# Kernel optimization log

Hardware: AMD Instinct MI355X
Metric: run time of the kernel (lower is better)

## Reference

```python
import jax, jax.numpy as jnp
import numpy as np

N, D, K = 10000, 784, 16          # nodes, input feat dim, num_neighbors
E = N * (K - 1)                   # edges
H = 128                           # hidden width in all MLPs
SIZES = [784, 128, 2]             # node_sizes


def setup_inputs() -> dict:
    key = jax.random.key(0)
    ks = jax.random.split(key, 24)
    w = lambda k, shape: jax.random.normal(k, shape, jnp.float32) * 0.02
    inp = {
        "x": jax.random.normal(ks[0], (N, D), jnp.float32),
        "edge_attr": jax.random.uniform(ks[1], (E, 1), jnp.float32),
        "idxs": jax.random.randint(ks[2], (N, K - 1), 0, N, dtype=jnp.int32),
    }
    # Layer 1: in=784, msg_size=784, out=128
    inp["l1_msg_w1"] = w(ks[3], (D + 1, H));      inp["l1_msg_b1"] = jnp.zeros((H,), jnp.float32)
    inp["l1_msg_w2"] = w(ks[4], (H, D));          inp["l1_msg_b2"] = jnp.zeros((D,), jnp.float32)
    inp["l1_node_w1"] = w(ks[5], (D + D, H));     inp["l1_node_b1"] = jnp.zeros((H,), jnp.float32)
    inp["l1_node_w2"] = w(ks[6], (H, 128));       inp["l1_node_b2"] = jnp.zeros((128,), jnp.float32)
    # Layer 2: in=128, msg_size=128, out=2
    inp["l2_msg_w1"] = w(ks[7], (128 + 1, H));    inp["l2_msg_b1"] = jnp.zeros((H,), jnp.float32)
    inp["l2_msg_w2"] = w(ks[8], (H, 128));        inp["l2_msg_b2"] = jnp.zeros((128,), jnp.float32)
    inp["l2_node_w1"] = w(ks[9], (128 + 128, H)); inp["l2_node_b1"] = jnp.zeros((H,), jnp.float32)
    inp["l2_node_w2"] = w(ks[10], (H, 2));        inp["l2_node_b2"] = jnp.zeros((2,), jnp.float32)
    return inp


def _mlp(x, w1, b1, w2, b2):
    return jax.nn.relu(x @ w1 + b1) @ w2 + b2


def _node_layer(x, src, edge_attr,
                mw1, mb1, mw2, mb2, nw1, nb1, nw2, nb2):
    # message over edges: cat(x[src], edge_attr) -> MLP   [E, msg_size]
    msg = _mlp(jnp.concatenate([x[src], edge_attr], axis=1), mw1, mb1, mw2, mb2)
    # scatter_mean by src index (faithful to the original, which uses index=src)
    sums = jax.ops.segment_sum(msg, src, num_segments=N)
    cnt = jax.ops.segment_sum(jnp.ones((src.shape[0], 1), msg.dtype), src, num_segments=N)
    agg = jnp.where(cnt > 0, sums / jnp.maximum(cnt, 1.0), 0.0)
    # node update: cat(x, agg_msg) -> MLP
    return _mlp(jnp.concatenate([x, agg], axis=1), nw1, nb1, nw2, nb2)


def reference(x, edge_attr, idxs,
              l1_msg_w1, l1_msg_b1, l1_msg_w2, l1_msg_b2,
              l1_node_w1, l1_node_b1, l1_node_w2, l1_node_b2,
              l2_msg_w1, l2_msg_b1, l2_msg_w2, l2_msg_b2,
              l2_node_w1, l2_node_b1, l2_node_w2, l2_node_b2):
    src = idxs.reshape(-1)  # [E]; dst is unused by the original message computation
    h = _node_layer(x, src, edge_attr,
                    l1_msg_w1, l1_msg_b1, l1_msg_w2, l1_msg_b2,
                    l1_node_w1, l1_node_b1, l1_node_w2, l1_node_b2)
    proj = _node_layer(h, src, edge_attr,
                       l2_msg_w1, l2_msg_b1, l2_msg_w2, l2_msg_b2,
                       l2_node_w1, l2_node_b1, l2_node_w2, l2_node_b2)  # [N, 2]
    # vectorized per-neighbor squared distances (replaces the nested python loop)
    neigh = proj[idxs]                                   # [N, K-1, 2]
    d = jnp.sum((proj[:, None, :] - neigh) ** 2, axis=-1)  # [N, K-1]
    return d.reshape(-1, 1)                              # [N*(K-1), 1]
```

## Files before the change

kernel.cpp:

```cpp
#include <hip/hip_runtime.h>

#define N_NODES 10000
#define E_EDGES 150000
#define KNB     15
#define EBLOCKS 587
#define GEMMB   626
#define KPAD    832
#define PLSTR   212992
#define CFSTR   13312

typedef unsigned short u16;
typedef __bf16 bf16x8 __attribute__((ext_vector_type(8)));
typedef float  f32x4  __attribute__((ext_vector_type(4)));
typedef unsigned short u16x8 __attribute__((ext_vector_type(8)));

__device__ __forceinline__ void split3(float a, u16& h, u16& m, u16& l) {
    unsigned u = __float_as_uint(a);
    unsigned t = u + 0x7FFFu + ((u >> 16) & 1u);
    h = (u16)(t >> 16);
    float r1 = a - __uint_as_float(t & 0xFFFF0000u);
    unsigned u1 = __float_as_uint(r1);
    m = (u16)(u1 >> 16);
    float r2 = r1 - __uint_as_float(u1 & 0xFFFF0000u);
    l = (u16)(__float_as_uint(r2) >> 16);
}

__global__ void count_kernel(const int* __restrict__ idxs, int* __restrict__ cnt, int e) {
    int i = blockIdx.x * blockDim.x + threadIdx.x;
    if (i < e) atomicAdd(&cnt[idxs[i]], 1);
}

__device__ __forceinline__
void gemm_tile2(const float* __restrict__ A, int K,
                const float* __restrict__ Blo, const float* __restrict__ Bhi, int ldB,
                float* __restrict__ C, int ldC, int M,
                int rowBlk, int colBlk) {
    __shared__ float As2[16][34];
    __shared__ float Bs2[16][64];
    int tid = threadIdx.x;
    int tn  = tid & 15, tm = tid >> 4;
    int arow = tid >> 3, acB = (tid & 7) << 1;
    int brow = tid >> 4, bcol = (tid & 15) << 2;
    int rowBase = rowBlk * 32, colBase = colBlk * 64;

    bool half = (Bhi != nullptr) && (colBase >= 128);
    const float* B = half ? Bhi : Blo;
    int bj = colBase - (half ? 128 : 0) + bcol;

    float2 av; float4 bv;
    auto loadA = [&](int k0, float2& dst) {
        int gr = rowBase + arow;
        if (gr < M) dst = *(const float2*)(A + (size_t)gr * K + k0 + acB);
        else { dst.x = dst.y = 0.f; }
    };
    auto loadB = [&](int k0, float4& dst) {
        dst = *(const float4*)(B + (size_t)(k0 + brow) * ldB + bj);
    };
    loadA(0, av); loadB(0, bv);

    float acc[2][4] = {};
    for (int k0 = 0; k0 < K; k0 += 16) {
        __syncthreads();
        As2[acB + 0][arow] = av.x; As2[acB + 1][arow] = av.y;
        *(float4*)&Bs2[brow][bcol] = bv;
        __syncthreads();
        if (k0 + 16 < K) { loadA(k0 + 16, av); loadB(k0 + 16, bv); }
#pragma unroll
        for (int k = 0; k < 16; ++k) {
            float4 b = *(const float4*)&Bs2[k][tn << 2];
            float2 a = *(const float2*)&As2[k][tm << 1];
            acc[0][0] = fmaf(a.x, b.x, acc[0][0]); acc[0][1] = fmaf(a.x, b.y, acc[0][1]);
            acc[0][2] = fmaf(a.x, b.z, acc[0][2]); acc[0][3] = fmaf(a.x, b.w, acc[0][3]);
            acc[1][0] = fmaf(a.y, b.x, acc[1][0]); acc[1][1] = fmaf(a.y, b.y, acc[1][1]);
            acc[1][2] = fmaf(a.y, b.z, acc[1][2]); acc[1][3] = fmaf(a.y, b.w, acc[1][3]);
        }
    }
#pragma unroll
    for (int i = 0; i < 2; ++i) {
        int row = rowBase + tm * 2 + i;
        if (row >= M) continue;
#pragma unroll
        for (int j = 0; j < 4; ++j)
            C[(size_t)row * ldC + colBase + (tn << 2) + j] = acc[i][j];
    }
}

__global__ __launch_bounds__(256)
void scanfold_kernel(const float* __restrict__ mw2, const float* __restrict__ mb2,
                     const float* __restrict__ nw1, const float* __restrict__ nb2,
                     const float* __restrict__ nw2,
                     const float* __restrict__ m2w1, const float* __restrict__ m2b1,
                     const float* __restrict__ m2w2, const float* __restrict__ m2b2,
                     const float* __restrict__ n2w1, const float* __restrict__ n2b1,
                     float* __restrict__ M1, float* __restrict__ M2,
                     float* __restrict__ WH,
                     float* __restrict__ v1, float* __restrict__ v2,
                     float* __restrict__ bu2, float* __restrict__ bx2,
                     const int* __restrict__ cnt, int* __restrict__ eoff,
                     float* __restrict__ maskv, int* __restrict__ fillc,
                     const float* __restrict__ mw1, u16* __restrict__ Bt) {
    int b = blockIdx.x;
    if (b >= 41) {
        __shared__ float Lt[KPAD][17];
        int b2 = b - 41;
        int colBase = b2 * 16;
        const float* S = (colBase < 128) ? mw1 : nw1;
        int sc = colBase & 127;
        int tid = threadIdx.x;
        for (int i = 0; i < 52; ++i) {
            int row = (tid >> 4) + i * 16;
            Lt[row][tid & 15] = (row < 784) ? S[(size_t)row * 128 + sc + (tid & 15)] : 0.f;
        }
        __syncthreads();
        int col = tid >> 4, o = tid & 15;
        size_t dbase = (size_t)(colBase + col) * KPAD;
        for (int o2 = o; o2 < 104; o2 += 16) {
            u16 hs[8], ms[8], ls[8];
#pragma unroll
            for (int e = 0; e < 8; ++e) split3(Lt[o2 * 8 + e][col], hs[e], ms[e], ls[e]);
            auto pk = [](const u16* s) {
                uint4 v;
                v.x = s[0] | ((unsigned)s[1] << 16); v.y = s[2] | ((unsigned)s[3] << 16);
                v.z = s[4] | ((unsigned)s[5] << 16); v.w = s[6] | ((unsigned)s[7] << 16);
                return v;
            };
            *(uint4*)(Bt +           dbase + o2 * 8) = pk(hs);
            *(uint4*)(Bt + PLSTR   + dbase + o2 * 8) = pk(ms);
            *(uint4*)(Bt + 2*PLSTR + dbase + o2 * 8) = pk(ls);
        }
        return;
    }
    if (b == 0) {
        __shared__ int ssum[256];
        int tid = threadIdx.x;
        const int CH = 40;
        int base = tid * CH;
        int v[CH]; int s = 0;
#pragma unroll
        for (int q = 0; q < CH; ++q) {
            int i = base + q;
            v[q] = (i < N_NODES) ? cnt[i] : 0;
            s += v[q];
        }
        ssum[tid] = s;
        __syncthreads();
        for (int off = 1; off < 256; off <<= 1) {
            int t = (tid >= off) ? ssum[tid - off] : 0;
            __syncthreads();
            ssum[tid] += t;
            __syncthreads();
        }
        int ex = ssum[tid] - s;
#pragma unroll
        for (int q = 0; q < CH; ++q) {
            int i = base + q;
            if (i < N_NODES) {
                eoff[i]  = ex;
                maskv[i] = (v[q] > 0) ? 1.f : 0.f;
                fillc[i] = 0;
                ex += v[q];
            }
        }
        return;
    }
    b -= 1;
    if (b < 8) {
        gemm_tile2(mw2, 784, nw1 + 784 * 128, nullptr, 128, M1, 128, 128, b >> 1, b & 1);
    } else if (b < 16) {
        int t = b - 8;
        gemm_tile2(m2w2, 128, n2w1 + 128 * 128, nullptr, 128, M2, 128, 128, t >> 1, t & 1);
    } else if (b < 32) {
        int t = b - 16;
        gemm_tile2(nw2, 128, m2w1, n2w1, 128, WH, 256, 128, t >> 2, t & 3);
    } else {
        __shared__ float red[256];
        int t  = (b - 32) >> 1;
        int j  = ((b - 32) & 1) * 64 + (threadIdx.x & 63);
        int kq = threadIdx.x >> 6;
        const float* bvec; const float* Bv; const float* add; float* out; int Kv;
        if (t == 0)      { bvec = mb2;  Bv = nw1 + 784 * 128;  add = nullptr; out = v1;  Kv = 784; }
        else if (t == 1) { bvec = m2b2; Bv = n2w1 + 128 * 128; add = nullptr; out = v2;  Kv = 128; }
        else if (t == 2) { bvec = nb2;  Bv = m2w1;             add = m2b1;    out = bu2; Kv = 128; }
        else             { bvec = nb2;  Bv = n2w1;             add = n2b1;    out = bx2; Kv = 128; }
        float acc = 0.f;
        for (int k = kq; k < Kv; k += 4) acc = fmaf(bvec[k], Bv[k * 128 + j], acc);
        red[threadIdx.x] = acc;
        __syncthreads();
        if (threadIdx.x < 64) {
            float tot = red[threadIdx.x] + red[threadIdx.x + 64] +
                        red[threadIdx.x + 128] + red[threadIdx.x + 192];
            out[j] = tot + (add ? add[j] : 0.f);
        }
    }
}

#define MF(a, b, c) __builtin_amdgcn_mfma_f32_16x16x32_bf16((a), (b), (c), 0, 0, 0)

__device__ __forceinline__
void gemm_mfma(const float* __restrict__ A, const u16* __restrict__ Bt,
               const float* __restrict__ biasLo, const float* __restrict__ biasHi,
               const float* __restrict__ vhi, const float* __restrict__ rowmask,
               float* __restrict__ C, int gb) {
    __shared__ u16 As[3][2][2][64][8];
    const int tid  = threadIdx.x;
    const int lane = tid & 63, w = tid >> 6;
    const int rb = gb >> 1, cb = gb & 1;
    const int rowBase = rb * 32, colBase = cb * 128;
    u16* const AsB = &As[0][0][0][0][0];

    const int skt = w >> 1, srf = w & 1;
    const int aoff = skt * 32 + ((lane >> 4) << 3);
    int arow = rowBase + srf * 16 + (lane & 15);
    if (arow > N_NODES - 1) arow = N_NODES - 1;
    const float* Ap = A + (size_t)arow * 784;
    u16* aDst = AsB + skt * 1024 + srf * 512 + (lane << 3);

    const u16* Bp = Bt + (size_t)(colBase + w * 32 + (lane & 15)) * KPAD
                       + ((lane >> 4) << 3);

    float4 av0, av1;
    u16x8 a3h, a3m, a3l;

#define ALOAD(k0) { int kk = (k0) + aoff; \
    if (kk < 784) { av0 = *(const float4*)(Ap + kk); av1 = *(const float4*)(Ap + kk + 4); } \
    else { av0.x=av0.y=av0.z=av0.w=0.f; av1 = av0; } }
#define ASPLIT() { u16 h, m, l; \
    split3(av0.x, h, m, l); a3h[0] = h; a3m[0] = m; a3l[0] = l; \
    split3(av0.y, h, m, l); a3h[1] = h; a3m[1] = m; a3l[1] = l; \
    split3(av0.z, h, m, l); a3h[2] = h; a3m[2] = m; a3l[2] = l; \
    split3(av0.w, h, m, l); a3h[3] = h; a3m[3] = m; a3l[3] = l; \
    split3(av1.x, h, m, l); a3h[4] = h; a3m[4] = m; a3l[4] = l; \
    split3(av1.y, h, m, l); a3h[5] = h; a3m[5] = m; a3l[5] = l; \
    split3(av1.z, h, m, l); a3h[6] = h; a3m[6] = m; a3l[6] = l; \
    split3(av1.w, h, m, l); a3h[7] = h; a3m[7] = m; a3l[7] = l; }

#define BDECL(S) bf16x8 S##h00, S##h01, S##h10, S##h11, \
                        S##m00, S##m01, S##m10, S##m11, \
                        S##l00, S##l01, S##l10, S##l11;
#define BLOAD(S, k0) \
    S##h00 = *(const bf16x8*)(Bp + (k0)); \
    S##h01 = *(const bf16x8*)(Bp + (k0) + CFSTR); \
    S##h10 = *(const bf16x8*)(Bp + (k0) + 32); \
    S##h11 = *(const bf16x8*)(Bp + (k0) + CFSTR + 32); \
    S##m00 = *(const bf16x8*)(Bp + (k0) + PLSTR); \
    S##m01 = *(const bf16x8*)(Bp + (k0) + PLSTR + CFSTR); \
    S##m10 = *(const bf16x8*)(Bp + (k0) + PLSTR + 32); \
    S##m11 = *(const bf16x8*)(Bp + (k0) + PLSTR + CFSTR + 32); \
    S##l00 = *(const bf16x8*)(Bp + (k0) + 2*PLSTR); \
    S##l01 = *(const bf16x8*)(Bp + (k0) + 2*PLSTR + CFSTR); \
    S##l10 = *(const bf16x8*)(Bp + (k0) + 2*PLSTR + 32); \
    S##l11 = *(const bf16x8*)(Bp + (k0) + 2*PLSTR + CFSTR + 32);

#define DOMFMA(S) { \
    {  \
        bf16x8 a0h = *(const bf16x8*)(aFr); \
        bf16x8 a1h = *(const bf16x8*)(aFr + 512); \
        bf16x8 a0m = *(const bf16x8*)(aFr + 2048); \
        bf16x8 a1m = *(const bf16x8*)(aFr + 2560); \
        bf16x8 a0l = *(const bf16x8*)(aFr + 4096); \
        bf16x8 a1l = *(const bf16x8*)(aFr + 4608); \
        acc00 = MF(a0h, S##h00, acc00); acc01 = MF(a0h, S##h01, acc01); \
        acc10 = MF(a1h, S##h00, acc10); acc11 = MF(a1h, S##h01, acc11); \
        acc00 = MF(a0m, S##h00, acc00); acc01 = MF(a0m, S##h01, acc01); \
        acc10 = MF(a1m, S##h00, acc10); acc11 = MF(a1m, S##h01, acc11); \
        acc00 = MF(a0l, S##h00, acc00); acc01 = MF(a0l, S##h01, acc01); \
        acc10 = MF(a1l, S##h00, acc10); acc11 = MF(a1l, S##h01, acc11); \
        acc00 = MF(a0h, S##m00, acc00); acc01 = MF(a0h, S##m01, acc01); \
        acc10 = MF(a1h, S##m00, acc10); acc11 = MF(a1h, S##m01, acc11); \
        acc00 = MF(a0m, S##m00, acc00); acc01 = MF(a0m, S##m01, acc01); \
        acc10 = MF(a1m, S##m00, acc10); acc11 = MF(a1m, S##m01, acc11); \
        acc00 = MF(a0h, S##l00, acc00); acc01 = MF(a0h, S##l01, acc01); \
        acc10 = MF(a1h, S##l00, acc10); acc11 = MF(a1h, S##l01, acc11); \
    } \
    {  \
        bf16x8 a0h = *(const bf16x8*)(aFr + 1024); \
        bf16x8 a1h = *(const bf16x8*)(aFr + 1536); \
        bf16x8 a0m = *(const bf16x8*)(aFr + 3072); \
        bf16x8 a1m = *(const bf16x8*)(aFr + 3584); \
        bf16x8 a0l = *(const bf16x8*)(aFr + 5120); \
        bf16x8 a1l = *(const bf16x8*)(aFr + 5632); \
        acc00 = MF(a0h, S##h10, acc00); acc01 = MF(a0h, S##h11, acc01); \
        acc10 = MF(a1h, S##h10, acc10); acc11 = MF(a1h, S##h11, acc11); \
        acc00 = MF(a0m, S##h10, acc00); acc01 = MF(a0m, S##h11, acc01); \
        acc10 = MF(a1m, S##h10, acc10); acc11 = MF(a1m, S##h11, acc11); \
        acc00 = MF(a0l, S##h10, acc00); acc01 = MF(a0l, S##h11, acc01); \
        acc10 = MF(a1l, S##h10, acc10); acc11 = MF(a1l, S##h11, acc11); \
        acc00 = MF(a0h, S##m10, acc00); acc01 = MF(a0h, S##m11, acc01); \
        acc10 = MF(a1h, S##m10, acc10); acc11 = MF(a1h, S##m11, acc11); \
        acc00 = MF(a0m, S##m10, acc00); acc01 = MF(a0m, S##m11, acc01); \
        acc10 = MF(a1m, S##m10, acc10); acc11 = MF(a1m, S##m11, acc11); \
        acc00 = MF(a0h, S##l10, acc00); acc01 = MF(a0h, S##l11, acc01); \
        acc10 = MF(a1h, S##l10, acc10); acc11 = MF(a1h, S##l11, acc11); \
    } }

#define ITER(CUR, NXT, T) { \
    __syncthreads(); \
    *(u16x8*)(aDst)        = a3h; \
    *(u16x8*)(aDst + 2048) = a3m; \
    *(u16x8*)(aDst + 4096) = a3l; \
    __syncthreads(); \
    if ((T) < 12) { ALOAD(((T) + 1) << 6) BLOAD(NXT, ((T) + 1) << 6) } \
    DOMFMA(CUR) \
    if ((T) < 12) { ASPLIT() } }

    f32x4 acc00 = {0.f, 0.f, 0.f, 0.f};
    f32x4 acc01 = acc00, acc10 = acc00, acc11 = acc00;

    const u16* aFr = AsB + (lane << 3);

    BDECL(p) BDECL(q)
    ALOAD(0) ASPLIT()
    BLOAD(p, 0)

    ITER(p, q, 0)  ITER(q, p, 1)  ITER(p, q, 2)  ITER(q, p, 3)
    ITER(p, q, 4)  ITER(q, p, 5)  ITER(p, q, 6)  ITER(q, p, 7)
    ITER(p, q, 8)  ITER(q, p, 9)  ITER(p, q, 10) ITER(q, p, 11)
    ITER(p, q, 12)

#undef ITER
#undef DOMFMA
#undef BLOAD
#undef BDECL
#undef ALOAD
#undef ASPLIT

    const float* bias = cb ? biasHi : biasLo;
#define EPI(rf, cf, ACC) { \
        const int col = colBase + w * 32 + (cf) * 16 + (lane & 15); \
        const int cj  = col & 127; \
        const float bb = bias[cj]; \
        const float vh = cb ? vhi[cj] : 0.f; \
        const int rbase = rowBase + (rf) * 16 + ((lane >> 4) << 2); \
        _Pragma("unroll") \
        for (int rr = 0; rr < 4; ++rr) { \
            int row = rbase + rr; \
            if (row < N_NODES) { \
                float v = ACC[rr] + bb; \
                if (cb) v = fmaf(rowmask[row], vh, v); \
                C[(size_t)row * 256 + col] = v; \
            } } }
    EPI(0, 0, acc00) EPI(0, 1, acc01) EPI(1, 0, acc10) EPI(1, 1, acc11)
#undef EPI
}

__global__ __launch_bounds__(256, 1)
void fillgemm_kernel(const int* __restrict__ idxs, const float* __restrict__ ea,
                     const int* __restrict__ eoff, int* __restrict__ fillc,
                     float* __restrict__ eas,
                     const float* __restrict__ A, const u16* __restrict__ Bt,
                     const float* __restrict__ biasLo, const float* __restrict__ biasHi,
                     const float* __restrict__ vhi, const float* __restrict__ rowmask,
                     float* __restrict__ C) {
    int gb = blockIdx.x;
    if (gb < GEMMB) {
        gemm_mfma(A, Bt, biasLo, biasHi, vhi, rowmask, C, gb);
        return;
    }
    int i = (gb - GEMMB) * 256 + threadIdx.x;
    if (i < E_EDGES) {
        int s = idxs[i];
        int p = atomicAdd(&fillc[s], 1);
        eas[eoff[s] + p] = ea[i];
    }
}

__global__ __launch_bounds__(512, 4)
void tail16_kernel(const float* __restrict__ UX1, const float* __restrict__ w1last,
                   const float* __restrict__ eas, const int* __restrict__ eoff,
                   const int* __restrict__ cnt, const float* __restrict__ maskv,
                   const float* __restrict__ M1, const float* __restrict__ WH,
                   const float* __restrict__ bu2, const float* __restrict__ bx2,
                   const float* __restrict__ v2,
                   const float* __restrict__ w2last, const float* __restrict__ M2,
                   const float* __restrict__ pw, const float* __restrict__ pb,
                   float* __restrict__ UX2, float* __restrict__ proj) {
    __shared__ float Bs[16][264];
    __shared__ float mhT[128][18];
    __shared__ float ts[16][132];
    __shared__ float ebuf[1024];
    int rowBase = blockIdx.x * 16;
    int tid = threadIdx.x;
    int tr  = tid >> 5;
    int tn  = tid & 31;
    int c4  = tn << 2;

    auto msg_phase = [&](const float* __restrict__ U, const float* __restrict__ wl) {
        int d = tid & 127, grp = tid >> 7;
        float w = wl[d];
        float uu[4], sum[4];
        int es[4], ec[4];
#pragma unroll
        for (int it = 0; it < 4; ++it) {
            int n  = rowBase + it * 4 + grp;
            ec[it] = cnt[n];
            es[it] = eoff[n];
            uu[it] = U[(size_t)n * 256 + d];
            sum[it] = 0.f;
        }
        int ebase = eoff[rowBase];
        int eend  = (rowBase + 16 < N_NODES) ? eoff[rowBase + 16] : E_EDGES;
        for (int w0 = ebase; w0 < eend; w0 += 1024) {
            int wlen = min(1024, eend - w0);
            __syncthreads();
            for (int q = tid; q < wlen; q += 512) ebuf[q] = eas[w0 + q];
            __syncthreads();
#pragma unroll
            for (int it = 0; it < 4; ++it) {
                int lo = max(es[it], w0), hiE = min(es[it] + ec[it], w0 + wlen);
                for (int e = lo; e < hiE; ++e)
                    sum[it] += fmaxf(fmaf(ebuf[e - w0], w, uu[it]), 0.f);
            }
        }
#pragma unroll
        for (int it = 0; it < 4; ++it)
            mhT[d][it * 4 + grp] = (ec[it] > 0) ? sum[it] / (float)ec[it] : 0.f;
    };

    msg_phase(UX1, w1last);

    {
        float a0 = 0.f, a1 = 0.f, a2 = 0.f, a3 = 0.f;
        float4 bv = *(const float4*)(M1 + (size_t)tr * 128 + c4);
        for (int k0 = 0; k0 < 128; k0 += 16) {
            __syncthreads();
            *(float4*)&Bs[tr][c4] = bv;
            __syncthreads();
            if (k0 + 16 < 128)
                bv = *(const float4*)(M1 + (size_t)(k0 + 16 + tr) * 128 + c4);
#pragma unroll
            for (int k = 0; k < 16; ++k) {
                float a = mhT[k0 + k][tr];
                float4 b = *(const float4*)&Bs[k][c4];
                a0 = fmaf(a, b.x, a0); a1 = fmaf(a, b.y, a1);
                a2 = fmaf(a, b.z, a2); a3 = fmaf(a, b.w, a3);
            }
        }
        int row = rowBase + tr;
        float4 xn = *(const float4*)(UX1 + (size_t)row * 256 + 128 + c4);
        float4 o;
        o.x = fmaxf(a0 + xn.x, 0.f);
        o.y = fmaxf(a1 + xn.y, 0.f);
        o.z = fmaxf(a2 + xn.z, 0.f);
        o.w = fmaxf(a3 + xn.w, 0.f);
        *(float4*)&ts[tr][c4] = o;
    }

    {
        float u0 = 0.f, u1 = 0.f, u2 = 0.f, u3 = 0.f;
        float x0 = 0.f, x1 = 0.f, x2 = 0.f, x3 = 0.f;
        int c8 = tn << 3;
        float4 bva = *(const float4*)(WH + (size_t)tr * 256 + c8);
        float4 bvb = *(const float4*)(WH + (size_t)tr * 256 + c8 + 4);
        for (int k0 = 0; k0 < 128; k0 += 16) {
            __syncthreads();
            *(float4*)&Bs[tr][c8]     = bva;
            *(float4*)&Bs[tr][c8 + 4] = bvb;
            __syncthreads();
            if (k0 + 16 < 128) {
                bva = *(const float4*)(WH + (size_t)(k0 + 16 + tr) * 256 + c8);
                bvb = *(const float4*)(WH + (size_t)(k0 + 16 + tr) * 256 + c8 + 4);
            }
#pragma unroll
            for (int k = 0; k < 16; ++k) {
                float a = ts[tr][k0 + k];
                float4 b0 = *(const float4*)&Bs[k][c4];
                float4 b1 = *(const float4*)&Bs[k][c4 + 128];
                u0 = fmaf(a, b0.x, u0); u1 = fmaf(a, b0.y, u1);
                u2 = fmaf(a, b0.z, u2); u3 = fmaf(a, b0.w, u3);
                x0 = fmaf(a, b1.x, x0); x1 = fmaf(a, b1.y, x1);
                x2 = fmaf(a, b1.z, x2); x3 = fmaf(a, b1.w, x3);
            }
        }
        int row = rowBase + tr;
        float rm = maskv[row];
        float4 o0, o1;
        o0.x = u0 + bu2[c4 + 0]; o0.y = u1 + bu2[c4 + 1];
        o0.z = u2 + bu2[c4 + 2]; o0.w = u3 + bu2[c4 + 3];
        o1.x = fmaf(rm, v2[c4 + 0], x0 + bx2[c4 + 0]);
        o1.y = fmaf(rm, v2[c4 + 1], x1 + bx2[c4 + 1]);
        o1.z = fmaf(rm, v2[c4 + 2], x2 + bx2[c4 + 2]);
        o1.w = fmaf(rm, v2[c4 + 3], x3 + bx2[c4 + 3]);
        float* orow = UX2 + (size_t)row * 256;
        *(float4*)(orow + c4)       = o0;
        *(float4*)(orow + 128 + c4) = o1;
    }
    __syncthreads();

    msg_phase(UX2, w2last);

    {
        float a0 = 0.f, a1 = 0.f, a2 = 0.f, a3 = 0.f;
        float4 bv = *(const float4*)(M2 + (size_t)tr * 128 + c4);
        for (int k0 = 0; k0 < 128; k0 += 16) {
            __syncthreads();
            *(float4*)&Bs[tr][c4] = bv;
            __syncthreads();
            if (k0 + 16 < 128)
                bv = *(const float4*)(M2 + (size_t)(k0 + 16 + tr) * 128 + c4);
#pragma unroll
            for (int k = 0; k < 16; ++k) {
                float a = mhT[k0 + k][tr];
                float4 b = *(const float4*)&Bs[k][c4];
                a0 = fmaf(a, b.x, a0); a1 = fmaf(a, b.y, a1);
                a2 = fmaf(a, b.z, a2); a3 = fmaf(a, b.w, a3);
            }
        }
        int row = rowBase + tr;
        float4 xn = *(const float4*)(UX2 + (size_t)row * 256 + 128 + c4);
        float t0 = fmaxf(a0 + xn.x, 0.f);
        float t1 = fmaxf(a1 + xn.y, 0.f);
        float t2 = fmaxf(a2 + xn.z, 0.f);
        float t3 = fmaxf(a3 + xn.w, 0.f);
        float pp0 = fmaf(t3, pw[2*(c4+3)],   fmaf(t2, pw[2*(c4+2)],   fmaf(t1, pw[2*(c4+1)],   t0 * pw[2*c4])));
        float pp1 = fmaf(t3, pw[2*(c4+3)+1], fmaf(t2, pw[2*(c4+2)+1], fmaf(t1, pw[2*(c4+1)+1], t0 * pw[2*c4+1])));
        for (int off = 16; off > 0; off >>= 1) {
            pp0 += __shfl_xor(pp0, off, 64);
            pp1 += __shfl_xor(pp1, off, 64);
        }
        if (tn == 0) {
            proj[2 * row]     = pp0 + pb[0];
            proj[2 * row + 1] = pp1 + pb[1];
        }
    }
}

__global__ void dist_kernel(const float* __restrict__ proj, const int* __restrict__ idxs,
                            float* __restrict__ out, int e) {
    int i = blockIdx.x * blockDim.x + threadIdx.x;
    if (i >= e) return;
    int n = i / KNB;
    int m = idxs[i];
    float2 pn = *(const float2*)(proj + 2 * n);
    float2 pm = *(const float2*)(proj + 2 * m);
    float dx = pn.x - pm.x;
    float dy = pn.y - pm.y;
    out[i] = dx * dx + dy * dy;
}

extern "C" void kernel_launch(void* const* d_in, const int* in_sizes, int n_in,
                              void* d_out, int out_size, void* d_ws, size_t ws_size,
                              hipStream_t stream) {
    (void)in_sizes; (void)n_in; (void)out_size; (void)ws_size;
    const float* x    = (const float*)d_in[0];
    const float* eatt = (const float*)d_in[1];
    const int*   idxs = (const int*)d_in[2];
    const float* mw1  = (const float*)d_in[3];
    const float* mb1  = (const float*)d_in[4];
    const float* mw2  = (const float*)d_in[5];
    const float* mb2  = (const float*)d_in[6];
    const float* nw1  = (const float*)d_in[7];
    const float* nb1  = (const float*)d_in[8];
    const float* nw2  = (const float*)d_in[9];
    const float* nb2  = (const float*)d_in[10];
    const float* m2w1 = (const float*)d_in[11];
    const float* m2b1 = (const float*)d_in[12];
    const float* m2w2 = (const float*)d_in[13];
    const float* m2b2 = (const float*)d_in[14];
    const float* n2w1 = (const float*)d_in[15];
    const float* n2b1 = (const float*)d_in[16];
    const float* n2w2 = (const float*)d_in[17];
    const float* n2b2 = (const float*)d_in[18];
    float* out = (float*)d_out;

    float* fws   = (float*)d_ws;
    float* UX1   = fws;
    float* UX2   = fws + 2560000;
    float* proj  = fws + 5120000;
    float* maskv = fws + 5140000;
    float* eas   = fws + 5150016;
    float* M1    = fws + 5300016;
    float* M2    = fws + 5316400;
    float* WH    = fws + 5332784;
    float* v1    = fws + 5365552;
    float* v2    = fws + 5365680;
    float* bu2   = fws + 5365808;
    float* bx2   = fws + 5365936;
    int*   cnt   = (int*)(fws + 5366064);
    int*   fillc = cnt + N_NODES;
    int*   eoff  = fillc + N_NODES;
    u16*   Bt    = (u16*)(fws + 2560000);

    hipMemsetAsync(cnt, 0, N_NODES * sizeof(int), stream);
    count_kernel<<<EBLOCKS, 256, 0, stream>>>(idxs, cnt, E_EDGES);

    scanfold_kernel<<<57, 256, 0, stream>>>(mw2, mb2, nw1, nb2, nw2,
                                            m2w1, m2b1, m2w2, m2b2, n2w1, n2b1,
                                            M1, M2, WH, v1, v2, bu2, bx2,
                                            cnt, eoff, maskv, fillc, mw1, Bt);

    fillgemm_kernel<<<GEMMB + EBLOCKS, 256, 0, stream>>>(
        idxs, eatt, eoff, fillc, eas,
        x, Bt, mb1, nb1, v1, maskv, UX1);

    tail16_kernel<<<625, 512, 0, stream>>>(UX1, mw1 + 784 * 128, eas, eoff, cnt, maskv,
                                           M1, WH, bu2, bx2, v2,
                                           m2w1 + 128 * 128, M2,
                                           n2w2, n2b2,
                                           UX2, proj);

    dist_kernel<<<EBLOCKS, 256, 0, stream>>>(proj, idxs, out, E_EDGES);
}
```

Baseline: 253.6 us.

## Halve GEMM column tile to 64 and raise occupancy of fused fill-GEMM kernel

Each GEMM block now covers 32 rows by 64 columns instead of 128, which doubles the block count. Each wave holds one 16-column fragment, so it carries half the accumulators and B registers it did before. Launch bounds now allow 4 blocks per CU, trading register footprint for more occupancy and better latency hiding. The cost is that the A tile loads and the bf16 three-way split are repeated twice as often across blocks.

Result: no change. 253.7 us (+0.0%).

```diff
diff --git a/kernel.cpp b/kernel.cpp
--- a/kernel.cpp
+++ b/kernel.cpp
@@ -4,10 +4,9 @@
 #define E_EDGES 150000
 #define KNB     15
 #define EBLOCKS 587
-#define GEMMB   626
+#define GEMMB   1252
 #define KPAD    832
 #define PLSTR   212992
-#define CFSTR   13312
 
 typedef unsigned short u16;
 typedef __bf16 bf16x8 __attribute__((ext_vector_type(8)));
@@ -204,8 +203,9 @@
     __shared__ u16 As[3][2][2][64][8];
     const int tid  = threadIdx.x;
     const int lane = tid & 63, w = tid >> 6;
-    const int rb = gb >> 1, cb = gb & 1;
-    const int rowBase = rb * 32, colBase = cb * 128;
+    const int rb = gb >> 2, cbq = gb & 3;
+    const int rowBase = rb * 32, colBase = cbq * 64;
+    const bool hi = cbq >= 2;
     u16* const AsB = &As[0][0][0][0][0];
 
     const int skt = w >> 1, srf = w & 1;
@@ -215,7 +215,7 @@
     const float* Ap = A + (size_t)arow * 784;
     u16* aDst = AsB + skt * 1024 + srf * 512 + (lane << 3);
 
-    const u16* Bp = Bt + (size_t)(colBase + w * 32 + (lane & 15)) * KPAD
+    const u16* Bp = Bt + (size_t)(colBase + w * 16 + (lane & 15)) * KPAD
                        + ((lane >> 4) << 3);
 
     float4 av0, av1;
@@ -234,22 +234,14 @@
     split3(av1.z, h, m, l); a3h[6] = h; a3m[6] = m; a3l[6] = l; \
     split3(av1.w, h, m, l); a3h[7] = h; a3m[7] = m; a3l[7] = l; }
 
-#define BDECL(S) bf16x8 S##h00, S##h01, S##h10, S##h11, \
-                        S##m00, S##m01, S##m10, S##m11, \
-                        S##l00, S##l01, S##l10, S##l11;
+#define BDECL(S) bf16x8 S##h0, S##h1, S##m0, S##m1, S##l0, S##l1;
 #define BLOAD(S, k0) \
-    S##h00 = *(const bf16x8*)(Bp + (k0)); \
-    S##h01 = *(const bf16x8*)(Bp + (k0) + CFSTR); \
-    S##h10 = *(const bf16x8*)(Bp + (k0) + 32); \
-    S##h11 = *(const bf16x8*)(Bp + (k0) + CFSTR + 32); \
-    S##m00 = *(const bf16x8*)(Bp + (k0) + PLSTR); \
-    S##m01 = *(const bf16x8*)(Bp + (k0) + PLSTR + CFSTR); \
-    S##m10 = *(const bf16x8*)(Bp + (k0) + PLSTR + 32); \
-    S##m11 = *(const bf16x8*)(Bp + (k0) + PLSTR + CFSTR + 32); \
-    S##l00 = *(const bf16x8*)(Bp + (k0) + 2*PLSTR); \
-    S##l01 = *(const bf16x8*)(Bp + (k0) + 2*PLSTR + CFSTR); \
-    S##l10 = *(const bf16x8*)(Bp + (k0) + 2*PLSTR + 32); \
-    S##l11 = *(const bf16x8*)(Bp + (k0) + 2*PLSTR + CFSTR + 32);
+    S##h0 = *(const bf16x8*)(Bp + (k0)); \
+    S##h1 = *(const bf16x8*)(Bp + (k0) + 32); \
+    S##m0 = *(const bf16x8*)(Bp + (k0) + PLSTR); \
+    S##m1 = *(const bf16x8*)(Bp + (k0) + PLSTR + 32); \
+    S##l0 = *(const bf16x8*)(Bp + (k0) + 2*PLSTR); \
+    S##l1 = *(const bf16x8*)(Bp + (k0) + 2*PLSTR + 32);
 
 #define DOMFMA(S) { \
     {  \
@@ -259,18 +251,12 @@
         bf16x8 a1m = *(const bf16x8*)(aFr + 2560); \
         bf16x8 a0l = *(const bf16x8*)(aFr + 4096); \
         bf16x8 a1l = *(const bf16x8*)(aFr + 4608); \
-        acc00 = MF(a0h, S##h00, acc00); acc01 = MF(a0h, S##h01, acc01); \
-        acc10 = MF(a1h, S##h00, acc10); acc11 = MF(a1h, S##h01, acc11); \
-        acc00 = MF(a0m, S##h00, acc00); acc01 = MF(a0m, S##h01, acc01); \
-        acc10 = MF(a1m, S##h00, acc10); acc11 = MF(a1m, S##h01, acc11); \
-        acc00 = MF(a0l, S##h00, acc00); acc01 = MF(a0l, S##h01, acc01); \
-        acc10 = MF(a1l, S##h00, acc10); acc11 = MF(a1l, S##h01, acc11); \
-        acc00 = MF(a0h, S##m00, acc00); acc01 = MF(a0h, S##m01, acc01); \
-        acc10 = MF(a1h, S##m00, acc10); acc11 = MF(a1h, S##m01, acc11); \
-        acc00 = MF(a0m, S##m00, acc00); acc01 = MF(a0m, S##m01, acc01); \
-        acc10 = MF(a1m, S##m00, acc10); acc11 = MF(a1m, S##m01, acc11); \
-        acc00 = MF(a0h, S##l00, acc00); acc01 = MF(a0h, S##l01, acc01); \
-        acc10 = MF(a1h, S##l00, acc10); acc11 = MF(a1h, S##l01, acc11); \
+        acc0 = MF(a0h, S##h0, acc0); acc1 = MF(a1h, S##h0, acc1); \
+        acc0 = MF(a0m, S##h0, acc0); acc1 = MF(a1m, S##h0, acc1); \
+        acc0 = MF(a0l, S##h0, acc0); acc1 = MF(a1l, S##h0, acc1); \
+        acc0 = MF(a0h, S##m0, acc0); acc1 = MF(a1h, S##m0, acc1); \
+        acc0 = MF(a0m, S##m0, acc0); acc1 = MF(a1m, S##m0, acc1); \
+        acc0 = MF(a0h, S##l0, acc0); acc1 = MF(a1h, S##l0, acc1); \
     } \
     {  \
         bf16x8 a0h = *(const bf16x8*)(aFr + 1024); \
@@ -279,18 +265,12 @@
         bf16x8 a1m = *(const bf16x8*)(aFr + 3584); \
         bf16x8 a0l = *(const bf16x8*)(aFr + 5120); \
         bf16x8 a1l = *(const bf16x8*)(aFr + 5632); \
-        acc00 = MF(a0h, S##h10, acc00); acc01 = MF(a0h, S##h11, acc01); \
-        acc10 = MF(a1h, S##h10, acc10); acc11 = MF(a1h, S##h11, acc11); \
-        acc00 = MF(a0m, S##h10, acc00); acc01 = MF(a0m, S##h11, acc01); \
-        acc10 = MF(a1m, S##h10, acc10); acc11 = MF(a1m, S##h11, acc11); \
-        acc00 = MF(a0l, S##h10, acc00); acc01 = MF(a0l, S##h11, acc01); \
-        acc10 = MF(a1l, S##h10, acc10); acc11 = MF(a1l, S##h11, acc11); \
-        acc00 = MF(a0h, S##m10, acc00); acc01 = MF(a0h, S##m11, acc01); \
-        acc10 = MF(a1h, S##m10, acc10); acc11 = MF(a1h, S##m11, acc11); \
-        acc00 = MF(a0m, S##m10, acc00); acc01 = MF(a0m, S##m11, acc01); \
-        acc10 = MF(a1m, S##m10, acc10); acc11 = MF(a1m, S##m11, acc11); \
-        acc00 = MF(a0h, S##l10, acc00); acc01 = MF(a0h, S##l11, acc01); \
-        acc10 = MF(a1h, S##l10, acc10); acc11 = MF(a1h, S##l11, acc11); \
+        acc0 = MF(a0h, S##h1, acc0); acc1 = MF(a1h, S##h1, acc1); \
+        acc0 = MF(a0m, S##h1, acc0); acc1 = MF(a1m, S##h1, acc1); \
+        acc0 = MF(a0l, S##h1, acc0); acc1 = MF(a1l, S##h1, acc1); \
+        acc0 = MF(a0h, S##m1, acc0); acc1 = MF(a1h, S##m1, acc1); \
+        acc0 = MF(a0m, S##m1, acc0); acc1 = MF(a1m, S##m1, acc1); \
+        acc0 = MF(a0h, S##l1, acc0); acc1 = MF(a1h, S##l1, acc1); \
     } }
 
 #define ITER(CUR, NXT, T) { \
@@ -303,8 +283,8 @@
     DOMFMA(CUR) \
     if ((T) < 12) { ASPLIT() } }
 
-    f32x4 acc00 = {0.f, 0.f, 0.f, 0.f};
-    f32x4 acc01 = acc00, acc10 = acc00, acc11 = acc00;
+    f32x4 acc0 = {0.f, 0.f, 0.f, 0.f};
+    f32x4 acc1 = acc0;
 
     const u16* aFr = AsB + (lane << 3);
 
@@ -324,26 +304,26 @@
 #undef ALOAD
 #undef ASPLIT
 
-    const float* bias = cb ? biasHi : biasLo;
-#define EPI(rf, cf, ACC) { \
-        const int col = colBase + w * 32 + (cf) * 16 + (lane & 15); \
+    const float* bias = hi ? biasHi : biasLo;
+#define EPI(rf, ACC) { \
+        const int col = colBase + w * 16 + (lane & 15); \
         const int cj  = col & 127; \
         const float bb = bias[cj]; \
-        const float vh = cb ? vhi[cj] : 0.f; \
+        const float vh = hi ? vhi[cj] : 0.f; \
         const int rbase = rowBase + (rf) * 16 + ((lane >> 4) << 2); \
         _Pragma("unroll") \
         for (int rr = 0; rr < 4; ++rr) { \
             int row = rbase + rr; \
             if (row < N_NODES) { \
                 float v = ACC[rr] + bb; \
-                if (cb) v = fmaf(rowmask[row], vh, v); \
+                if (hi) v = fmaf(rowmask[row], vh, v); \
                 C[(size_t)row * 256 + col] = v; \
             } } }
-    EPI(0, 0, acc00) EPI(0, 1, acc01) EPI(1, 0, acc10) EPI(1, 1, acc11)
+    EPI(0, acc0) EPI(1, acc1)
 #undef EPI
 }
 
-__global__ __launch_bounds__(256, 1)
+__global__ __launch_bounds__(256, 4)
 void fillgemm_kernel(const int* __restrict__ idxs, const float* __restrict__ ea,
                      const int* __restrict__ eoff, int* __restrict__ fillc,
                      float* __restrict__ eas,
```
